# Optimization experiments

Hardware: AMD Instinct MI355X
Metric: run time of the kernel (lower is better)

The kernel has to match this reference:

```python
import jax, jax.numpy as jnp
import numpy as np

N_U, N_I, D = 30000, 15000, 64
L = 2                 # propagation layers (self.l)
TEMP = 0.2
LAMBDA1, LAMBDA2 = 0.2, 1e-7
H, F = 4, 16          # GAT heads x per-head dim; H*F == D
NEG_SLOPE = 0.2
AVG_DEG = 16
B = 2048


def setup_inputs() -> dict:
    key = jax.random.key(0)
    ks = jax.random.split(key, 10)
    rng = np.random.default_rng(0)
    E_u_0 = jax.random.normal(ks[0], (N_U, D), jnp.float32) * 0.1
    E_i_0 = jax.random.normal(ks[1], (N_I, D), jnp.float32) * 0.1
    # sparse normalized bipartite adjacency (adj_norm) as an edge list
    nnz = N_U * AVG_DEG
    u_idx = np.repeat(np.arange(N_U), AVG_DEG)
    i_idx = rng.integers(0, N_I, nnz)
    deg_u = np.bincount(u_idx, minlength=N_U)
    deg_i = np.maximum(np.bincount(i_idx, minlength=N_I), 1)
    vals = (1.0 / np.sqrt(deg_u[u_idx] * deg_i[i_idx])).astype(np.float32)
    # GAT graph on n_u+n_i nodes: bipartite edges both directions + self-loops
    n = N_U + N_I
    src = np.concatenate([u_idx, i_idx + N_U, np.arange(n)]).astype(np.int32)
    dst = np.concatenate([i_idx + N_U, u_idx, np.arange(n)]).astype(np.int32)
    # GAT parameters (fresh each forward in original, so just random)
    W = jax.random.normal(ks[2], (D, H * F), jnp.float32) / np.sqrt(D)
    attn_l = jax.random.normal(ks[3], (H, F), jnp.float32) * 0.1
    attn_r = jax.random.normal(ks[4], (H, F), jnp.float32) * 0.1
    uids = jax.random.randint(ks[5], (B,), 0, N_U, jnp.int32)
    iids = jax.random.randint(ks[6], (B,), 0, N_I, jnp.int32)
    pos = jax.random.randint(ks[7], (B,), 0, N_I, jnp.int32)
    neg = jax.random.randint(ks[8], (B,), 0, N_I, jnp.int32)
    return dict(E_u_0=E_u_0, E_i_0=E_i_0, adj_vals=jnp.asarray(vals),
                W=W, attn_l=attn_l, attn_r=attn_r,
                u_idx=jnp.asarray(u_idx, jnp.int32), i_idx=jnp.asarray(i_idx, jnp.int32),
                src=jnp.asarray(src), dst=jnp.asarray(dst),
                uids=uids, iids=iids, pos=pos, neg=neg)


def gat_layer(h, src, dst, W, attn_l, attn_r, n_nodes):
    # GATConv: project, per-edge attention, neighborhood softmax, scatter-agg
    feat = (h @ W).reshape(-1, H, F)                      # [N,H,F]
    el = (feat * attn_l).sum(-1)                          # [N,H]
    er = (feat * attn_r).sum(-1)                          # [N,H]
    e = jax.nn.leaky_relu(el[src] + er[dst], NEG_SLOPE)   # [E,H]
    e_max = jax.ops.segment_max(e, dst, num_segments=n_nodes)
    a = jnp.exp(e - e_max[dst])
    denom = jax.ops.segment_sum(a, dst, num_segments=n_nodes)
    a = a / denom[dst]                                    # self-loops => denom>0
    out = jax.ops.segment_sum(a[:, :, None] * feat[src], dst, num_segments=n_nodes)
    return jax.nn.elu(out.reshape(-1, H * F))             # [N,D]


def _forward(E_u_0, E_i_0, adj_vals, W, attn_l, attn_r,
             u_idx, i_idx, src, dst, uids, iids, pos, neg):
    n = N_U + N_I
    Eu, Ei = E_u_0, E_i_0
    sum_Eu, sum_Ei = E_u_0, E_i_0
    sum_Gu, sum_Gi = E_u_0, E_i_0
    for _ in range(L):
        # LightGCN spmm propagation: Z_u = A @ E_i, Z_i = A.T @ E_u
        Zu = jax.ops.segment_sum(adj_vals[:, None] * Ei[i_idx], u_idx, num_segments=N_U)
        Zi = jax.ops.segment_sum(adj_vals[:, None] * Eu[u_idx], i_idx, num_segments=N_I)
        ls1 = gat_layer(jnp.concatenate([Eu, Ei], 0), src, dst, W, attn_l, attn_r, n)
        Gu, Gi = ls1[:N_U], ls1[N_U:]
        Eu, Ei = Zu + Eu, Zi + Ei
        sum_Eu = sum_Eu + Eu
        sum_Ei = sum_Ei + Ei
        sum_Gu = sum_Gu + Gu
        sum_Gi = sum_Gi + Gi
    log_eps = jnp.float32(np.log(1e-8))
    # InfoNCE: log(sum(exp(s)) + 1e-8) == logaddexp(logsumexp(s), log(1e-8))
    lse_u = jax.scipy.special.logsumexp(sum_Gu[uids] @ sum_Eu.T / TEMP, axis=1)
    lse_i = jax.scipy.special.logsumexp(sum_Gi[iids] @ sum_Ei.T / TEMP, axis=1)
    neg_score = jnp.logaddexp(lse_u, log_eps).mean() + jnp.logaddexp(lse_i, log_eps).mean()
    pos_score = ((sum_Gu[uids] * sum_Eu[uids]).sum(1) / TEMP).mean() \
              + ((sum_Gi[iids] * sum_Ei[iids]).sum(1) / TEMP).mean()
    loss_s = -pos_score + neg_score
    # BPR loss
    u_emb = sum_Eu[uids]
    diff = (u_emb * sum_Ei[pos]).sum(-1) - (u_emb * sum_Ei[neg]).sum(-1)
    loss_r = -jax.nn.log_sigmoid(diff).mean()
    # L2 reg over nn.Parameters (E_u_0, E_i_0 only)
    loss_reg = LAMBDA2 * ((E_u_0 ** 2).sum() + (E_i_0 ** 2).sum())
    loss = loss_r + LAMBDA1 * loss_s + loss_reg
    return loss, loss_r, LAMBDA1 * loss_s


def reference(E_u_0, E_i_0, adj_vals, W, attn_l, attn_r,
              u_idx, i_idx, src, dst, uids, iids, pos, neg):
    return _forward(E_u_0, E_i_0, adj_vals, W, attn_l, attn_r,
                    u_idx, i_idx, src, dst, uids, iids, pos, neg)
```

## Files before the change

### kernel.cpp

```cpp
#include <hip/hip_runtime.h>
#include <math.h>

#define N_U 30000
#define N_I 15000
#define N_TOT 45000
#define D 64
#define NNZ 480000
#define B 2048
#define INV_TEMP 5.0f
#define LOG_EPS -18.420680743952367f
#define NEG_SLOPE 0.2f
#define LAMBDA1 0.2f
#define LAMBDA2 1e-7f

#define NSP 128
#define RSP_U 235
#define RSP_I 118
#define PAD_U 30016
#define PAD_I 15040
#define SCALE_LOG2 7.2134752044448170f
#define LN2F 0.6931471805599453f

typedef __attribute__((ext_vector_type(8))) short short8;
typedef __attribute__((ext_vector_type(4))) float f32x4;

__device__ inline float wred(float v) {
#pragma unroll
  for (int o = 32; o > 0; o >>= 1) v += __shfl_down(v, o, 64);
  return v;
}

__device__ inline float leaky(float v) { return (v >= 0.f) ? v : NEG_SLOPE * v; }

__device__ inline void atomMaxF(float* a, float v) {
  if (v >= 0.f) atomicMax((int*)a, __float_as_int(v));
  else atomicMin((unsigned int*)a, __float_as_uint(v));
}

__device__ inline unsigned short f2bf(float x) {
  unsigned u = __float_as_uint(x);
  unsigned r = u + 0x7FFFu + ((u >> 16) & 1u);
  return (unsigned short)(r >> 16);
}
__device__ inline float bf2f(unsigned short h) {
  return __uint_as_float(((unsigned)h) << 16);
}

__global__ void k_init(const float* __restrict__ Eu0, const float* __restrict__ Ei0,
                       float* fU, float* fI,
                       unsigned short* gU, unsigned short* gI,
                       float* sEu, float* sEi,
                       float* sGu, float* sGi, int* deg, float* acc) {
  int t = blockIdx.x * 256 + threadIdx.x;
  if (t < 16) acc[t] = (t >= 8) ? -INFINITY : 0.f;
  if (t < N_I) deg[t] = 0;
  if (t < N_U * D) {
    int n = t >> 6, c = t & 63;
    float v = Eu0[t];
    fU[(size_t)n * 128 + c] = v;
    gU[(size_t)n * 128 + c] = f2bf(v);
    sEu[t] = v; sGu[t] = v;
  } else if (t < N_TOT * D) {
    int j = t - N_U * D;
    int n = j >> 6, c = j & 63;
    float v = Ei0[j];
    fI[(size_t)n * 128 + c] = v;
    gI[(size_t)n * 128 + c] = f2bf(v);
    sEi[j] = v; sGi[j] = v;
  }
}

__global__ void k_deg(const int* __restrict__ ii, int* deg) {
  int e = blockIdx.x * 256 + threadIdx.x;
  if (e < NNZ) atomicAdd(&deg[ii[e]], 1);
}

__global__ void k_scan(const int* __restrict__ deg, int* rowptr, int* cursor) {
  __shared__ int tsum[1024];
  const int CHUNK = 15;
  int tid = threadIdx.x;
  int base = tid * CHUNK;
  int s = 0;
#pragma unroll
  for (int k = 0; k < CHUNK; k++) {
    int idx = base + k;
    s += (idx < N_I) ? deg[idx] : 0;
  }
  tsum[tid] = s;
  __syncthreads();
  for (int o = 1; o < 1024; o <<= 1) {
    int x = (tid >= o) ? tsum[tid - o] : 0;
    __syncthreads();
    tsum[tid] += x;
    __syncthreads();
  }
  int excl = tsum[tid] - s;
#pragma unroll
  for (int k = 0; k < CHUNK; k++) {
    int idx = base + k;
    if (idx < N_I) {
      rowptr[idx] = excl;
      cursor[idx] = excl;
      excl += deg[idx];
    }
  }
  if (tid == 1023) rowptr[N_I] = tsum[1023];
}

__global__ void k_fill(const int* __restrict__ ii, const float* __restrict__ vals,
                       int* cursor, int* u_srt, float* v_srt) {
  int e = blockIdx.x * 256 + threadIdx.x;
  if (e < NNZ) {
    int pos = atomicAdd(&cursor[ii[e]], 1);
    u_srt[pos] = e >> 4;
    v_srt[pos] = vals[e];
  }
}

__global__ void k_feat(float* __restrict__ fU, float* __restrict__ fI,
                       unsigned short* __restrict__ gU, unsigned short* __restrict__ gI,
                       const float* __restrict__ W, const float* __restrict__ al,
                       const float* __restrict__ ar,
                       float* __restrict__ el, float* __restrict__ er) {
  __shared__ float Ws[64 * 64];
  __shared__ float hs[16][64];
  int tid = threadIdx.x;
  for (int t = tid; t < 1024; t += 256) ((float4*)Ws)[t] = ((const float4*)W)[t];
  int g = tid >> 6, c = tid & 63;
  int n0 = blockIdx.x * 16 + g * 4;
  float* rows[4];
  unsigned short* grows[4];
#pragma unroll
  for (int j = 0; j < 4; j++) {
    int node = n0 + j;
    rows[j] = nullptr; grows[j] = nullptr;
    if (node < N_TOT) {
      if (node < N_U) {
        rows[j] = fU + (size_t)node * 128;
        grows[j] = gU + (size_t)node * 128;
      } else {
        rows[j] = fI + (size_t)(node - N_U) * 128;
        grows[j] = gI + (size_t)(node - N_U) * 128;
      }
      hs[g * 4 + j][c] = rows[j][c];
    }
  }
  __syncthreads();
  float a0 = 0.f, a1 = 0.f, a2 = 0.f, a3 = 0.f;
#pragma unroll 8
  for (int k = 0; k < 64; ++k) {
    float w = Ws[k * 64 + c];
    a0 = fmaf(hs[g * 4 + 0][k], w, a0);
    a1 = fmaf(hs[g * 4 + 1][k], w, a1);
    a2 = fmaf(hs[g * 4 + 2][k], w, a2);
    a3 = fmaf(hs[g * 4 + 3][k], w, a3);
  }
  float accs[4] = {a0, a1, a2, a3};
  float alc = al[c], arc = ar[c];
#pragma unroll
  for (int j = 0; j < 4; j++) {
    int node = n0 + j;
    if (node >= N_TOT) continue;
    rows[j][64 + c] = accs[j];
    grows[j][64 + c] = f2bf(accs[j]);
    float pl = accs[j] * alc;
    float pr = accs[j] * arc;
#pragma unroll
    for (int o = 8; o >= 1; o >>= 1) {
      pl += __shfl_down(pl, o, 16);
      pr += __shfl_down(pr, o, 16);
    }
    if ((c & 15) == 0) {
      el[node * 4 + (c >> 4)] = pl;
      er[node * 4 + (c >> 4)] = pr;
    }
  }
}

__global__ void k_elmax(const float* __restrict__ el, float* __restrict__ dst) {
  __shared__ float red[4][4];
  int tid = threadIdx.x;
  int lane = tid & 63, wv = tid >> 6;
  float mx = -INFINITY;
  for (int t = blockIdx.x * 256 + tid; t < N_TOT * 4; t += 64 * 256)
    mx = fmaxf(mx, el[t]);
#pragma unroll
  for (int o = 4; o < 64; o <<= 1) mx = fmaxf(mx, __shfl_xor(mx, o, 64));
  if (lane < 4) red[wv][lane] = mx;
  __syncthreads();
  if (tid < 4) {
    float m2 = fmaxf(fmaxf(red[0][tid], red[1][tid]), fmaxf(red[2][tid], red[3][tid]));
    atomMaxF(dst + tid, m2);
  }
}

__global__ void k_layer(const float* __restrict__ fU_cur, const float* __restrict__ fI_cur,
                        const unsigned short* __restrict__ gU_cur,
                        const unsigned short* __restrict__ gI_cur,
                        const float* __restrict__ el, const float* __restrict__ er,
                        const float* __restrict__ vals, const int* __restrict__ ii,
                        const int* __restrict__ rowptr, const int* __restrict__ u_srt,
                        const float* __restrict__ v_srt,
                        const float* __restrict__ elmx,
                        float* __restrict__ fU_nxt, float* __restrict__ fI_nxt,
                        unsigned short* __restrict__ gU_nxt, unsigned short* __restrict__ gI_nxt,
                        float* __restrict__ sEu, float* __restrict__ sEi,
                        float* __restrict__ sGu, float* __restrict__ sGi,
                        unsigned short* __restrict__ EuH, unsigned short* __restrict__ EuL,
                        unsigned short* __restrict__ EiH, unsigned short* __restrict__ EiL,
                        float* __restrict__ normU, float* __restrict__ normI) {
  int t = blockIdx.x * 256 + threadIdx.x;
  int node = t >> 6, c = t & 63;
  if (node >= N_TOT) return;
  int h = c >> 4;

  if (node < N_U) {
    int u = node;
    float eru = er[u * 4 + h];
    float m = leaky(elmx[h] + eru);
    const float* selfrow = fU_cur + (size_t)u * 128;
    float aself = __expf(leaky(el[u * 4 + h] + eru) - m);

    int idx[16]; float vv[16];
#pragma unroll
    for (int k = 0; k < 16; k++) { idx[k] = ii[u * 16 + k]; vv[k] = vals[u * 16 + k]; }
    float av[16];
#pragma unroll
    for (int k = 0; k < 16; k++)
      av[k] = __expf(leaky(el[(idx[k] + N_U) * 4 + h] + eru) - m);

    float den = aself;
#pragma unroll
    for (int k = 0; k < 16; k++) den += av[k];

    float o0 = aself * selfrow[64 + c], o1 = 0.f;
    float z0 = 0.f, z1 = 0.f;
#pragma unroll
    for (int k = 0; k < 16; k += 2) {
      const unsigned short* rA = gI_cur + (size_t)idx[k] * 128;
      const unsigned short* rB = gI_cur + (size_t)idx[k + 1] * 128;
      float eA = bf2f(rA[c]), fA = bf2f(rA[64 + c]);
      float eB = bf2f(rB[c]), fB = bf2f(rB[64 + c]);
      z0 = fmaf(vv[k], eA, z0);
      z1 = fmaf(vv[k + 1], eB, z1);
      o0 = fmaf(av[k], fA, o0);
      o1 = fmaf(av[k + 1], fB, o1);
    }
    float o = (o0 + o1) / den;
    float g = (o > 0.f) ? o : expm1f(o);
    float e_new = selfrow[c] + z0 + z1;
    fU_nxt[(size_t)u * 128 + c] = e_new;
    gU_nxt[(size_t)u * 128 + c] = f2bf(e_new);
    size_t off = (size_t)u * D + c;
    float s_final = sEu[off] + e_new;
    sEu[off] = s_final;
    sGu[off] += g;
    if (EuH) {
      unsigned short hi = f2bf(s_final);
      EuH[off] = hi;
      EuL[off] = f2bf(s_final - bf2f(hi));
      float n2 = wred(s_final * s_final);
      if (c == 0) normU[u] = n2;
    }
  } else {
    int i = node - N_U;
    float eri = er[node * 4 + h];
    float m = leaky(elmx[h] + eri);
    const float* selfrow = fI_cur + (size_t)i * 128;
    float aself = __expf(leaky(el[node * 4 + h] + eri) - m);
    float den0 = aself, den1 = 0.f;
    float o0 = aself * selfrow[64 + c], o1 = 0.f;
    float z0 = 0.f, z1 = 0.f;
    int r0 = rowptr[i], r1 = rowptr[i + 1];
    int r = r0;
    for (; r + 3 < r1; r += 4) {
      int u0 = u_srt[r], u1 = u_srt[r + 1], u2 = u_srt[r + 2], u3 = u_srt[r + 3];
      float v0 = v_srt[r], v1 = v_srt[r + 1], v2 = v_srt[r + 2], v3 = v_srt[r + 3];
      float a0 = __expf(leaky(el[u0 * 4 + h] + eri) - m);
      float a1 = __expf(leaky(el[u1 * 4 + h] + eri) - m);
      float a2 = __expf(leaky(el[u2 * 4 + h] + eri) - m);
      float a3 = __expf(leaky(el[u3 * 4 + h] + eri) - m);
      const unsigned short* R0 = gU_cur + (size_t)u0 * 128;
      const unsigned short* R1 = gU_cur + (size_t)u1 * 128;
      const unsigned short* R2 = gU_cur + (size_t)u2 * 128;
      const unsigned short* R3 = gU_cur + (size_t)u3 * 128;
      float e0 = bf2f(R0[c]), f0 = bf2f(R0[64 + c]);
      float e1 = bf2f(R1[c]), f1 = bf2f(R1[64 + c]);
      float e2 = bf2f(R2[c]), f2 = bf2f(R2[64 + c]);
      float e3 = bf2f(R3[c]), f3 = bf2f(R3[64 + c]);
      z0 = fmaf(v0, e0, z0); z1 = fmaf(v1, e1, z1);
      z0 = fmaf(v2, e2, z0); z1 = fmaf(v3, e3, z1);
      den0 += a0 + a2; den1 += a1 + a3;
      o0 = fmaf(a0, f0, o0); o1 = fmaf(a1, f1, o1);
      o0 = fmaf(a2, f2, o0); o1 = fmaf(a3, f3, o1);
    }
    for (; r < r1; r++) {
      int u0 = u_srt[r];
      float v0 = v_srt[r];
      float a0 = __expf(leaky(el[u0 * 4 + h] + eri) - m);
      const unsigned short* R0 = gU_cur + (size_t)u0 * 128;
      float e0 = bf2f(R0[c]), f0 = bf2f(R0[64 + c]);
      z0 = fmaf(v0, e0, z0);
      den0 += a0;
      o0 = fmaf(a0, f0, o0);
    }
    float o = (o0 + o1) / (den0 + den1);
    float g = (o > 0.f) ? o : expm1f(o);
    float e_new = selfrow[c] + z0 + z1;
    fI_nxt[(size_t)i * 128 + c] = e_new;
    gI_nxt[(size_t)i * 128 + c] = f2bf(e_new);
    size_t off = (size_t)i * D + c;
    float s_final = sEi[off] + e_new;
    sEi[off] = s_final;
    sGi[off] += g;
    if (EiH) {
      unsigned short hi = f2bf(s_final);
      EiH[off] = hi;
      EiL[off] = f2bf(s_final - bf2f(hi));
      float n2 = wred(s_final * s_final);
      if (c == 0) normI[i] = n2;
    }
  }
}

__global__ void k_normreg(const float* __restrict__ nU, const float* __restrict__ nI,
                          const float* __restrict__ Eu0, const float* __restrict__ Ei0,
                          float* __restrict__ acc) {
  __shared__ float red[4][3];
  int tid = threadIdx.x;
  int lane = tid & 63, wv = tid >> 6;
  float mu = 0.f, mi = 0.f, s = 0.f;
  for (int t = blockIdx.x * 256 + tid; t < N_U; t += 128 * 256) mu = fmaxf(mu, nU[t]);
  for (int t = blockIdx.x * 256 + tid; t < N_I; t += 128 * 256) mi = fmaxf(mi, nI[t]);
  const float4* A = (const float4*)Eu0;
  const float4* Bp = (const float4*)Ei0;
  const int nA = N_U * 16, nTot = N_TOT * 16;
  for (int t = blockIdx.x * 256 + tid; t < nTot; t += 128 * 256) {
    float4 v = (t < nA) ? A[t] : Bp[t - nA];
    s += v.x * v.x + v.y * v.y + v.z * v.z + v.w * v.w;
  }
#pragma unroll
  for (int o = 32; o > 0; o >>= 1) {
    mu = fmaxf(mu, __shfl_down(mu, o, 64));
    mi = fmaxf(mi, __shfl_down(mi, o, 64));
    s += __shfl_down(s, o, 64);
  }
  if (lane == 0) { red[wv][0] = mu; red[wv][1] = mi; red[wv][2] = s; }
  __syncthreads();
  if (tid == 0) {
    float a = fmaxf(fmaxf(red[0][0], red[1][0]), fmaxf(red[2][0], red[3][0]));
    float b = fmaxf(fmaxf(red[0][1], red[1][1]), fmaxf(red[2][1], red[3][1]));
    float ssum = red[0][2] + red[1][2] + red[2][2] + red[3][2];
    atomMaxF(acc + 6, a);
    atomMaxF(acc + 7, b);
    unsafeAtomicAdd(acc + 5, ssum);
  }
}

__global__ void k_cvt_q(const float* __restrict__ sGu, const float* __restrict__ sGi,
                        const int* __restrict__ uids, const int* __restrict__ iids,
                        unsigned short* __restrict__ QuH, unsigned short* __restrict__ QuL,
                        unsigned short* __restrict__ QiH, unsigned short* __restrict__ QiL,
                        const float* __restrict__ acc,
                        float* __restrict__ M0u, float* __restrict__ M0i) {
  int lane = threadIdx.x & 63, wv = threadIdx.x >> 6;
  int row = blockIdx.x * 4 + wv;
  int side = row >> 11;
  int b = row & (B - 1);
  int id = side ? iids[b] : uids[b];
  float x = (side ? sGi : sGu)[(size_t)id * 64 + lane] * SCALE_LOG2;
  unsigned short hi = f2bf(x);
  unsigned short lo = f2bf(x - bf2f(hi));
  if (side) { QiH[(size_t)b * 64 + lane] = hi; QiL[(size_t)b * 64 + lane] = lo; }
  else      { QuH[(size_t)b * 64 + lane] = hi; QuL[(size_t)b * 64 + lane] = lo; }
  float n2 = wred(x * x);
  if (lane == 0) {
    float en2 = side ? acc[7] : acc[6];
    float M0 = sqrtf(n2) * sqrtf(en2) * 1.01f + 1.0f;
    (side ? M0i : M0u)[b] = M0;
  }
}

__global__ __launch_bounds__(256, 2) void k_lse_mfma(
    const unsigned short* __restrict__ QuH, const unsigned short* __restrict__ QuL,
    const unsigned short* __restrict__ EuHp, const unsigned short* __restrict__ EuLp,
    const unsigned short* __restrict__ QiH, const unsigned short* __restrict__ QiL,
    const unsigned short* __restrict__ EiHp, const unsigned short* __restrict__ EiLp,
    const float* __restrict__ M0u, const float* __restrict__ M0i,
    float* __restrict__ psU, float* __restrict__ psI) {
  int z = blockIdx.z;
  const unsigned short* Qhi = z ? QiH : QuH;
  const unsigned short* Qlo = z ? QiL : QuL;
  const unsigned short* Ehi = z ? EiHp : EuHp;
  const unsigned short* Elo = z ? EiLp : EuLp;
  const float* M0arr = z ? M0i : M0u;
  float* part_s = z ? psI : psU;
  int n_rows = z ? N_I : N_U;
  int rows_per_split = z ? RSP_I : RSP_U;

  int tid = threadIdx.x;
  int wave = tid >> 6, lane = tid & 63;
  int l15 = lane & 15, quad = lane >> 4;
  int qbase = (blockIdx.x * 4 + wave) * 128;
  int split = blockIdx.y;
  int row0 = split * rows_per_split;
  int row_end = min(row0 + rows_per_split, n_rows);
  int rows = row_end - row0; if (rows < 0) rows = 0;
  int total = (rows + 15) >> 4;
  int ntail = rows & 15;

  float ss[8][4];
#pragma unroll
  for (int t = 0; t < 8; t++)
#pragma unroll
    for (int g = 0; g < 4; g++) ss[t][g] = 0.f;

  if (total > 0) {
    short8 ah[8][2], al[8][2];
#pragma unroll
    for (int t = 0; t < 8; t++)
#pragma unroll
      for (int c = 0; c < 2; c++) {
        size_t idx = (size_t)(qbase + t * 16 + l15) * 64 + c * 32 + quad * 8;
        ah[t][c] = *(const short8*)(Qhi + idx);
        al[t][c] = *(const short8*)(Qlo + idx);
      }

    f32x4 cinit[8];
#pragma unroll
    for (int t = 0; t < 8; t++)
#pragma unroll
      for (int g = 0; g < 4; g++)
        cinit[t][g] = -M0arr[qbase + t * 16 + quad * 4 + g];

    const unsigned short* ph = Ehi + (size_t)(row0 + l15) * 64 + quad * 8;
    const unsigned short* pl = Elo + (size_t)(row0 + l15) * 64 + quad * 8;

    short8 cb0 = *(const short8*)(ph);
    short8 cb1 = *(const short8*)(ph + 32);
    short8 cb2 = *(const short8*)(pl);
    short8 cb3 = *(const short8*)(pl + 32);
    ph += 1024; pl += 1024;

    for (int it = 0; it < total - 1; it++) {
      short8 nb0 = *(const short8*)(ph);
      short8 nb1 = *(const short8*)(ph + 32);
      short8 nb2 = *(const short8*)(pl);
      short8 nb3 = *(const short8*)(pl + 32);
      ph += 1024; pl += 1024;
#pragma unroll
      for (int t = 0; t < 8; t++) {
        f32x4 acc = cinit[t];
        acc = __builtin_amdgcn_mfma_f32_16x16x32_bf16(ah[t][0], cb0, acc, 0, 0, 0);
        acc = __builtin_amdgcn_mfma_f32_16x16x32_bf16(ah[t][1], cb1, acc, 0, 0, 0);
        acc = __builtin_amdgcn_mfma_f32_16x16x32_bf16(al[t][0], cb0, acc, 0, 0, 0);
        acc = __builtin_amdgcn_mfma_f32_16x16x32_bf16(al[t][1], cb1, acc, 0, 0, 0);
        acc = __builtin_amdgcn_mfma_f32_16x16x32_bf16(ah[t][0], cb2, acc, 0, 0, 0);
        acc = __builtin_amdgcn_mfma_f32_16x16x32_bf16(ah[t][1], cb3, acc, 0, 0, 0);
#pragma unroll
        for (int g = 0; g < 4; g++)
          ss[t][g] += exp2f(acc[g]);
      }
      cb0 = nb0; cb1 = nb1; cb2 = nb2; cb3 = nb3;
    }
    {
      bool valid = (ntail == 0) || (l15 < ntail);
#pragma unroll
      for (int t = 0; t < 8; t++) {
        f32x4 acc = cinit[t];
        acc = __builtin_amdgcn_mfma_f32_16x16x32_bf16(ah[t][0], cb0, acc, 0, 0, 0);
        acc = __builtin_amdgcn_mfma_f32_16x16x32_bf16(ah[t][1], cb1, acc, 0, 0, 0);
        acc = __builtin_amdgcn_mfma_f32_16x16x32_bf16(al[t][0], cb0, acc, 0, 0, 0);
        acc = __builtin_amdgcn_mfma_f32_16x16x32_bf16(al[t][1], cb1, acc, 0, 0, 0);
        acc = __builtin_amdgcn_mfma_f32_16x16x32_bf16(ah[t][0], cb2, acc, 0, 0, 0);
        acc = __builtin_amdgcn_mfma_f32_16x16x32_bf16(ah[t][1], cb3, acc, 0, 0, 0);
#pragma unroll
        for (int g = 0; g < 4; g++) {
          float e = exp2f(acc[g]);
          ss[t][g] += valid ? e : 0.f;
        }
      }
    }
  }

#pragma unroll
  for (int off = 1; off < 16; off <<= 1) {
#pragma unroll
    for (int t = 0; t < 8; t++)
#pragma unroll
      for (int g = 0; g < 4; g++)
        ss[t][g] += __shfl_xor(ss[t][g], off, 64);
  }

  if (l15 == 0) {
#pragma unroll
    for (int t = 0; t < 8; t++)
#pragma unroll
      for (int g = 0; g < 4; g++) {
        int q = qbase + t * 16 + quad * 4 + g;
        part_s[(size_t)split * B + q] = ss[t][g];
      }
  }
}

__global__ void k_small(const float* __restrict__ sEu, const float* __restrict__ sEi,
                        const float* __restrict__ sGu, const float* __restrict__ sGi,
                        const int* __restrict__ uids, const int* __restrict__ iids,
                        const int* __restrict__ pos, const int* __restrict__ neg,
                        const float* __restrict__ psU, const float* __restrict__ psI,
                        const float* __restrict__ M0u, const float* __restrict__ M0i,
                        float* acc) {
  int b = blockIdx.x * 256 + threadIdx.x;
  float du = 0.f, di = 0.f, nu = 0.f, ni = 0.f, bpr = 0.f;
  if (b < B) {
    float su = 0.f, si = 0.f;
    for (int s2 = 0; s2 < NSP; s2++) su += psU[(size_t)s2 * B + b];
    for (int s2 = 0; s2 < NSP; s2++) si += psI[(size_t)s2 * B + b];
    float lseu = M0u[b] * LN2F + logf(su);
    float lsei = M0i[b] * LN2F + logf(si);
    nu = fmaxf(lseu, LOG_EPS) + log1pf(expf(-fabsf(lseu - LOG_EPS)));
    ni = fmaxf(lsei, LOG_EPS) + log1pf(expf(-fabsf(lsei - LOG_EPS)));

    int u = uids[b], it = iids[b], p = pos[b], ng = neg[b];
    const float4* gu = (const float4*)(sGu + (size_t)u * D);
    const float4* eu = (const float4*)(sEu + (size_t)u * D);
    const float4* gi = (const float4*)(sGi + (size_t)it * D);
    const float4* ei = (const float4*)(sEi + (size_t)it * D);
    const float4* ep = (const float4*)(sEi + (size_t)p * D);
    const float4* en = (const float4*)(sEi + (size_t)ng * D);
    float diff = 0.f;
#pragma unroll
    for (int k = 0; k < 16; k++) {
      float4 a = gu[k], b4 = eu[k];
      du += a.x * b4.x + a.y * b4.y + a.z * b4.z + a.w * b4.w;
      float4 c = gi[k], d4 = ei[k];
      di += c.x * d4.x + c.y * d4.y + c.z * d4.z + c.w * d4.w;
      float4 e = ep[k], f = en[k];
      diff += b4.x * (e.x - f.x) + b4.y * (e.y - f.y) + b4.z * (e.z - f.z) + b4.w * (e.w - f.w);
    }
    bpr = (diff > 0.f) ? log1pf(expf(-diff)) : (-diff + log1pf(expf(diff)));
  }
  du = wred(du); di = wred(di); nu = wred(nu); ni = wred(ni); bpr = wred(bpr);
  if ((threadIdx.x & 63) == 0) {
    unsafeAtomicAdd(acc + 0, du);
    unsafeAtomicAdd(acc + 1, di);
    unsafeAtomicAdd(acc + 2, nu);
    unsafeAtomicAdd(acc + 3, ni);
    unsafeAtomicAdd(acc + 4, bpr);
  }
}

__global__ void k_final(const float* __restrict__ acc, float* __restrict__ out) {
  float pos_score = (acc[0] + acc[1]) * (INV_TEMP / (float)B);
  float neg_score = (acc[2] + acc[3]) / (float)B;
  float loss_s = neg_score - pos_score;
  float loss_r = acc[4] / (float)B;
  float reg = LAMBDA2 * acc[5];
  out[0] = loss_r + LAMBDA1 * loss_s + reg;
  out[1] = loss_r;
  out[2] = LAMBDA1 * loss_s;
}

extern "C" void kernel_launch(void* const* d_in, const int* in_sizes, int n_in,
                              void* d_out, int out_size, void* d_ws, size_t ws_size,
                              hipStream_t stream) {
  const float* Eu0  = (const float*)d_in[0];
  const float* Ei0  = (const float*)d_in[1];
  const float* vals = (const float*)d_in[2];
  const float* W    = (const float*)d_in[3];
  const float* al   = (const float*)d_in[4];
  const float* ar   = (const float*)d_in[5];
  const int* ii     = (const int*)d_in[7];
  const int* uids   = (const int*)d_in[10];
  const int* iids   = (const int*)d_in[11];
  const int* pos    = (const int*)d_in[12];
  const int* neg    = (const int*)d_in[13];
  float* out = (float*)d_out;

  char* base = (char*)d_ws;
  size_t off = 0;
  auto alloc = [&](size_t bytes) -> void* {
    void* p = base + off;
    off = (off + bytes + 255) & ~(size_t)255;
    return p;
  };
  float* fU_a = (float*)alloc((size_t)N_U * 128 * 4);
  float* fU_b = (float*)alloc((size_t)N_U * 128 * 4);
  float* fI_a = (float*)alloc((size_t)N_I * 128 * 4);
  float* fI_b = (float*)alloc((size_t)N_I * 128 * 4);
  unsigned short* gU_a = (unsigned short*)alloc((size_t)N_U * 128 * 2);
  unsigned short* gU_b = (unsigned short*)alloc((size_t)N_U * 128 * 2);
  unsigned short* gI_a = (unsigned short*)alloc((size_t)N_I * 128 * 2);
  unsigned short* gI_b = (unsigned short*)alloc((size_t)N_I * 128 * 2);
  float* sEu  = (float*)alloc((size_t)N_U * D * 4);
  float* sEi  = (float*)alloc((size_t)N_I * D * 4);
  float* sGu  = (float*)alloc((size_t)N_U * D * 4);
  float* sGi  = (float*)alloc((size_t)N_I * D * 4);
  float* el   = (float*)alloc((size_t)N_TOT * 4 * 4);
  float* er   = (float*)alloc((size_t)N_TOT * 4 * 4);
  float* psU  = (float*)alloc((size_t)B * NSP * 4);
  float* psI  = (float*)alloc((size_t)B * NSP * 4);
  float* M0u  = (float*)alloc((size_t)B * 4);
  float* M0i  = (float*)alloc((size_t)B * 4);
  float* normU= (float*)alloc((size_t)N_U * 4);
  float* normI= (float*)alloc((size_t)N_I * 4);
  float* acc  = (float*)alloc(16 * 4);
  int* deg    = (int*)alloc((size_t)N_I * 4);
  int* cursor = (int*)alloc((size_t)N_I * 4);
  int* rowptr = (int*)alloc((size_t)(N_I + 1) * 4);
  int* u_srt  = (int*)alloc((size_t)NNZ * 4);
  float* v_srt= (float*)alloc((size_t)NNZ * 4);
  unsigned short* EuH = (unsigned short*)alloc((size_t)PAD_U * 64 * 2);
  unsigned short* EuL = (unsigned short*)alloc((size_t)PAD_U * 64 * 2);
  unsigned short* EiH = (unsigned short*)alloc((size_t)PAD_I * 64 * 2);
  unsigned short* EiL = (unsigned short*)alloc((size_t)PAD_I * 64 * 2);
  unsigned short* QuH = (unsigned short*)alloc((size_t)B * 64 * 2);
  unsigned short* QuL = (unsigned short*)alloc((size_t)B * 64 * 2);
  unsigned short* QiH = (unsigned short*)alloc((size_t)B * 64 * 2);
  unsigned short* QiL = (unsigned short*)alloc((size_t)B * 64 * 2);

  k_init<<<(N_TOT * D + 255) / 256, 256, 0, stream>>>(Eu0, Ei0, fU_a, fI_a, gU_a, gI_a,
                                                      sEu, sEi, sGu, sGi, deg, acc);
  k_deg<<<(NNZ + 255) / 256, 256, 0, stream>>>(ii, deg);
  k_scan<<<1, 1024, 0, stream>>>(deg, rowptr, cursor);
  k_fill<<<(NNZ + 255) / 256, 256, 0, stream>>>(ii, vals, cursor, u_srt, v_srt);

  float* cu = fU_a; float* ci = fI_a;
  float* nu = fU_b; float* ni = fI_b;
  unsigned short* gcu = gU_a; unsigned short* gci = gI_a;
  unsigned short* gnu = gU_b; unsigned short* gni = gI_b;
  for (int l = 0; l < 2; ++l) {
    float* elmx = acc + 8 + 4 * l;
    bool last = (l == 1);
    k_feat<<<(N_TOT + 15) / 16, 256, 0, stream>>>(cu, ci, gcu, gci, W, al, ar, el, er);
    k_elmax<<<64, 256, 0, stream>>>(el, elmx);
    k_layer<<<(N_TOT * D) / 256, 256, 0, stream>>>(
        cu, ci, gcu, gci, el, er, vals, ii, rowptr, u_srt, v_srt, elmx,
        nu, ni, gnu, gni, sEu, sEi, sGu, sGi,
        last ? EuH : nullptr, last ? EuL : nullptr,
        last ? EiH : nullptr, last ? EiL : nullptr,
        normU, normI);
    float* t1 = cu; cu = nu; nu = t1;
    float* t2 = ci; ci = ni; ni = t2;
    unsigned short* t3 = gcu; gcu = gnu; gnu = t3;
    unsigned short* t4 = gci; gci = gni; gni = t4;
  }

  k_normreg<<<128, 256, 0, stream>>>(normU, normI, Eu0, Ei0, acc);
  k_cvt_q<<<(2 * B) / 4, 256, 0, stream>>>(sGu, sGi, uids, iids, QuH, QuL, QiH, QiL, acc, M0u, M0i);
  k_lse_mfma<<<dim3(B / 512, NSP, 2), 256, 0, stream>>>(QuH, QuL, EuH, EuL,
                                                        QiH, QiL, EiH, EiL,
                                                        M0u, M0i, psU, psI);
  k_small<<<B / 256, 256, 0, stream>>>(sEu, sEi, sGu, sGi, uids, iids, pos, neg,
                                       psU, psI, M0u, M0i, acc);
  k_final<<<1, 1, 0, stream>>>(acc, out);
}
```

Before: 427.2 us.

## Precompute per-edge attention weights and interleave bf16 embedding/feature rows

Adds a k_att kernel that computes the exponentiated leaky attention scores once per edge and head, instead of having all 16 lanes of each head recompute them inside k_layer. It also interleaves the bf16 embedding and projected-feature values in the gather buffers, so each lane fetches both with one 32-bit load. The cost is an extra launch per layer, a row_i array, and two NNZ×4 float buffers (about 15 MB) that are written and then reread.

```diff
diff --git a/kernel.cpp b/kernel.cpp
--- a/kernel.cpp
+++ b/kernel.cpp
@@ -58,14 +58,14 @@
     int n = t >> 6, c = t & 63;
     float v = Eu0[t];
     fU[(size_t)n * 128 + c] = v;
-    gU[(size_t)n * 128 + c] = f2bf(v);
+    gU[(size_t)n * 128 + 2 * c] = f2bf(v);
     sEu[t] = v; sGu[t] = v;
   } else if (t < N_TOT * D) {
     int j = t - N_U * D;
     int n = j >> 6, c = j & 63;
     float v = Ei0[j];
     fI[(size_t)n * 128 + c] = v;
-    gI[(size_t)n * 128 + c] = f2bf(v);
+    gI[(size_t)n * 128 + 2 * c] = f2bf(v);
     sEi[j] = v; sGi[j] = v;
   }
 }
@@ -108,12 +108,14 @@
 }
 
 __global__ void k_fill(const int* __restrict__ ii, const float* __restrict__ vals,
-                       int* cursor, int* u_srt, float* v_srt) {
+                       int* cursor, int* u_srt, float* v_srt, int* row_i) {
   int e = blockIdx.x * 256 + threadIdx.x;
   if (e < NNZ) {
-    int pos = atomicAdd(&cursor[ii[e]], 1);
+    int i = ii[e];
+    int pos = atomicAdd(&cursor[i], 1);
     u_srt[pos] = e >> 4;
     v_srt[pos] = vals[e];
+    row_i[pos] = i;
   }
 }
 
@@ -162,7 +164,7 @@
     int node = n0 + j;
     if (node >= N_TOT) continue;
     rows[j][64 + c] = accs[j];
-    grows[j][64 + c] = f2bf(accs[j]);
+    grows[j][2 * c + 1] = f2bf(accs[j]);
     float pl = accs[j] * alc;
     float pr = accs[j] * arc;
 #pragma unroll
@@ -194,6 +196,27 @@
   }
 }
 
+__global__ void k_att(const float* __restrict__ el, const float* __restrict__ er,
+                      const int* __restrict__ ii, const int* __restrict__ u_srt,
+                      const int* __restrict__ row_i, const float* __restrict__ elmx,
+                      float* __restrict__ av_u, float* __restrict__ av_i) {
+  int t = blockIdx.x * 256 + threadIdx.x;
+  int h = t & 3;
+  if (t < NNZ * 4) {
+    int e = t >> 2;
+    int u = e >> 4;
+    float eru = er[u * 4 + h];
+    float m = leaky(elmx[h] + eru);
+    av_u[t] = __expf(leaky(el[(ii[e] + N_U) * 4 + h] + eru) - m);
+  } else if (t < 2 * NNZ * 4) {
+    int r = (t - NNZ * 4) >> 2;
+    int i = row_i[r];
+    float eri = er[(i + N_U) * 4 + h];
+    float m = leaky(elmx[h] + eri);
+    av_i[(size_t)r * 4 + h] = __expf(leaky(el[u_srt[r] * 4 + h] + eri) - m);
+  }
+}
+
 __global__ void k_layer(const float* __restrict__ fU_cur, const float* __restrict__ fI_cur,
                         const unsigned short* __restrict__ gU_cur,
                         const unsigned short* __restrict__ gI_cur,
@@ -201,6 +224,7 @@
                         const float* __restrict__ vals, const int* __restrict__ ii,
                         const int* __restrict__ rowptr, const int* __restrict__ u_srt,
                         const float* __restrict__ v_srt,
+                        const float* __restrict__ av_u, const float* __restrict__ av_i,
                         const float* __restrict__ elmx,
                         float* __restrict__ fU_nxt, float* __restrict__ fI_nxt,
                         unsigned short* __restrict__ gU_nxt, unsigned short* __restrict__ gI_nxt,
@@ -227,7 +251,7 @@
     float av[16];
 #pragma unroll
     for (int k = 0; k < 16; k++)
-      av[k] = __expf(leaky(el[(idx[k] + N_U) * 4 + h] + eru) - m);
+      av[k] = av_u[(size_t)(u * 16 + k) * 4 + h];
 
     float den = aself;
 #pragma unroll
@@ -237,10 +261,10 @@
     float z0 = 0.f, z1 = 0.f;
 #pragma unroll
     for (int k = 0; k < 16; k += 2) {
-      const unsigned short* rA = gI_cur + (size_t)idx[k] * 128;
-      const unsigned short* rB = gI_cur + (size_t)idx[k + 1] * 128;
-      float eA = bf2f(rA[c]), fA = bf2f(rA[64 + c]);
-      float eB = bf2f(rB[c]), fB = bf2f(rB[64 + c]);
+      unsigned wA = *(const unsigned*)(gI_cur + (size_t)idx[k] * 128 + 2 * c);
+      unsigned wB = *(const unsigned*)(gI_cur + (size_t)idx[k + 1] * 128 + 2 * c);
+      float eA = __uint_as_float(wA << 16), fA = __uint_as_float(wA & 0xFFFF0000u);
+      float eB = __uint_as_float(wB << 16), fB = __uint_as_float(wB & 0xFFFF0000u);
       z0 = fmaf(vv[k], eA, z0);
       z1 = fmaf(vv[k + 1], eB, z1);
       o0 = fmaf(av[k], fA, o0);
@@ -250,7 +274,7 @@
     float g = (o > 0.f) ? o : expm1f(o);
     float e_new = selfrow[c] + z0 + z1;
     fU_nxt[(size_t)u * 128 + c] = e_new;
-    gU_nxt[(size_t)u * 128 + c] = f2bf(e_new);
+    gU_nxt[(size_t)u * 128 + 2 * c] = f2bf(e_new);
     size_t off = (size_t)u * D + c;
     float s_final = sEu[off] + e_new;
     sEu[off] = s_final;
@@ -276,18 +300,18 @@
     for (; r + 3 < r1; r += 4) {
       int u0 = u_srt[r], u1 = u_srt[r + 1], u2 = u_srt[r + 2], u3 = u_srt[r + 3];
       float v0 = v_srt[r], v1 = v_srt[r + 1], v2 = v_srt[r + 2], v3 = v_srt[r + 3];
-      float a0 = __expf(leaky(el[u0 * 4 + h] + eri) - m);
-      float a1 = __expf(leaky(el[u1 * 4 + h] + eri) - m);
-      float a2 = __expf(leaky(el[u2 * 4 + h] + eri) - m);
-      float a3 = __expf(leaky(el[u3 * 4 + h] + eri) - m);
-      const unsigned short* R0 = gU_cur + (size_t)u0 * 128;
-      const unsigned short* R1 = gU_cur + (size_t)u1 * 128;
-      const unsigned short* R2 = gU_cur + (size_t)u2 * 128;
-      const unsigned short* R3 = gU_cur + (size_t)u3 * 128;
-      float e0 = bf2f(R0[c]), f0 = bf2f(R0[64 + c]);
-      float e1 = bf2f(R1[c]), f1 = bf2f(R1[64 + c]);
-      float e2 = bf2f(R2[c]), f2 = bf2f(R2[64 + c]);
-      float e3 = bf2f(R3[c]), f3 = bf2f(R3[64 + c]);
+      float a0 = av_i[(size_t)r * 4 + h];
+      float a1 = av_i[(size_t)(r + 1) * 4 + h];
+      float a2 = av_i[(size_t)(r + 2) * 4 + h];
+      float a3 = av_i[(size_t)(r + 3) * 4 + h];
+      unsigned w0 = *(const unsigned*)(gU_cur + (size_t)u0 * 128 + 2 * c);
+      unsigned w1 = *(const unsigned*)(gU_cur + (size_t)u1 * 128 + 2 * c);
+      unsigned w2 = *(const unsigned*)(gU_cur + (size_t)u2 * 128 + 2 * c);
+      unsigned w3 = *(const unsigned*)(gU_cur + (size_t)u3 * 128 + 2 * c);
+      float e0 = __uint_as_float(w0 << 16), f0 = __uint_as_float(w0 & 0xFFFF0000u);
+      float e1 = __uint_as_float(w1 << 16), f1 = __uint_as_float(w1 & 0xFFFF0000u);
+      float e2 = __uint_as_float(w2 << 16), f2 = __uint_as_float(w2 & 0xFFFF0000u);
+      float e3 = __uint_as_float(w3 << 16), f3 = __uint_as_float(w3 & 0xFFFF0000u);
       z0 = fmaf(v0, e0, z0); z1 = fmaf(v1, e1, z1);
       z0 = fmaf(v2, e2, z0); z1 = fmaf(v3, e3, z1);
       den0 += a0 + a2; den1 += a1 + a3;
@@ -297,9 +321,9 @@
     for (; r < r1; r++) {
       int u0 = u_srt[r];
       float v0 = v_srt[r];
-      float a0 = __expf(leaky(el[u0 * 4 + h] + eri) - m);
-      const unsigned short* R0 = gU_cur + (size_t)u0 * 128;
-      float e0 = bf2f(R0[c]), f0 = bf2f(R0[64 + c]);
+      float a0 = av_i[(size_t)r * 4 + h];
+      unsigned w0 = *(const unsigned*)(gU_cur + (size_t)u0 * 128 + 2 * c);
+      float e0 = __uint_as_float(w0 << 16), f0 = __uint_as_float(w0 & 0xFFFF0000u);
       z0 = fmaf(v0, e0, z0);
       den0 += a0;
       o0 = fmaf(a0, f0, o0);
@@ -308,7 +332,7 @@
     float g = (o > 0.f) ? o : expm1f(o);
     float e_new = selfrow[c] + z0 + z1;
     fI_nxt[(size_t)i * 128 + c] = e_new;
-    gI_nxt[(size_t)i * 128 + c] = f2bf(e_new);
+    gI_nxt[(size_t)i * 128 + 2 * c] = f2bf(e_new);
     size_t off = (size_t)i * D + c;
     float s_final = sEi[off] + e_new;
     sEi[off] = s_final;
@@ -610,6 +634,9 @@
   int* rowptr = (int*)alloc((size_t)(N_I + 1) * 4);
   int* u_srt  = (int*)alloc((size_t)NNZ * 4);
   float* v_srt= (float*)alloc((size_t)NNZ * 4);
+  int* row_i  = (int*)alloc((size_t)NNZ * 4);
+  float* av_u = (float*)alloc((size_t)NNZ * 4 * 4);
+  float* av_i = (float*)alloc((size_t)NNZ * 4 * 4);
   unsigned short* EuH = (unsigned short*)alloc((size_t)PAD_U * 64 * 2);
   unsigned short* EuL = (unsigned short*)alloc((size_t)PAD_U * 64 * 2);
   unsigned short* EiH = (unsigned short*)alloc((size_t)PAD_I * 64 * 2);
@@ -623,7 +650,7 @@
                                                       sEu, sEi, sGu, sGi, deg, acc);
   k_deg<<<(NNZ + 255) / 256, 256, 0, stream>>>(ii, deg);
   k_scan<<<1, 1024, 0, stream>>>(deg, rowptr, cursor);
-  k_fill<<<(NNZ + 255) / 256, 256, 0, stream>>>(ii, vals, cursor, u_srt, v_srt);
+  k_fill<<<(NNZ + 255) / 256, 256, 0, stream>>>(ii, vals, cursor, u_srt, v_srt, row_i);
 
   float* cu = fU_a; float* ci = fI_a;
   float* nu = fU_b; float* ni = fI_b;
@@ -634,8 +661,10 @@
     bool last = (l == 1);
     k_feat<<<(N_TOT + 15) / 16, 256, 0, stream>>>(cu, ci, gcu, gci, W, al, ar, el, er);
     k_elmax<<<64, 256, 0, stream>>>(el, elmx);
+    k_att<<<(2 * NNZ * 4 + 255) / 256, 256, 0, stream>>>(el, er, ii, u_srt, row_i, elmx,
+                                                         av_u, av_i);
     k_layer<<<(N_TOT * D) / 256, 256, 0, stream>>>(
-        cu, ci, gcu, gci, el, er, vals, ii, rowptr, u_srt, v_srt, elmx,
+        cu, ci, gcu, gci, el, er, vals, ii, rowptr, u_srt, v_srt, av_u, av_i, elmx,
         nu, ni, gnu, gni, sEu, sEi, sGu, sGi,
         last ? EuH : nullptr, last ? EuL : nullptr,
         last ? EiH : nullptr, last ? EiL : nullptr,
```

Result: slower. 437.5 us (+2.4%).
